# Optimization experiments

Hardware: AMD Instinct MI355X
Metric: run time of the kernel (lower is better)

The kernel has to match this reference:

```python
import jax, jax.numpy as jnp
import numpy as np

N_NODES = 50000
N_EDGES = 500000
F_IN = 16      # node feature dim F
F_OUT = 16     # channels F_
E_FEAT = 8     # edge feature dim
HIDDEN = 32    # kernel_network hidden size


def _glorot(key, shape):
    fan_in, fan_out = shape[0], shape[1]
    lim = np.sqrt(6.0 / (fan_in + fan_out)).astype(np.float32)
    return jax.random.uniform(key, shape, jnp.float32, -lim, lim)


def setup_inputs() -> dict:
    key = jax.random.key(0)
    ks = jax.random.split(key, 8)
    x = jax.random.normal(ks[0], (N_NODES, F_IN), jnp.float32)
    e = jax.random.uniform(ks[1], (N_EDGES, E_FEAT), jnp.float32)
    idx_i = jax.random.randint(ks[2], (N_EDGES,), 0, N_NODES, jnp.int32)  # targets
    idx_j = jax.random.randint(ks[3], (N_EDGES,), 0, N_NODES, jnp.int32)  # sources
    W1 = _glorot(ks[4], (E_FEAT, HIDDEN))
    b1 = jnp.zeros((HIDDEN,), jnp.float32)
    W2 = _glorot(ks[5], (HIDDEN, F_OUT * F_IN))
    b2 = jnp.zeros((F_OUT * F_IN,), jnp.float32)
    root_kernel = _glorot(ks[6], (F_IN, F_OUT))
    bias = jnp.zeros((F_OUT,), jnp.float32)
    return {"x": x, "e": e, "idx_i": idx_i, "idx_j": idx_j,
            "W1": W1, "b1": b1, "W2": W2, "b2": b2,
            "root_kernel": root_kernel, "bias": bias}


def reference(x, e, idx_i, idx_j, W1, b1, W2, b2, root_kernel, bias):
    # Edge-conditioned filter-generating network (MLP, relu hidden, linear out)
    h = jax.nn.relu(e @ W1 + b1)                       # [E, HIDDEN]
    kern = (h @ W2 + b2).reshape(-1, F_IN, F_OUT)      # [E, F, F_]
    # gather source node features, per-edge matmul, scatter-add to targets
    msg = jnp.einsum('ef,efc->ec', x[idx_j], kern)     # [E, F_]
    out = jax.ops.segment_sum(msg, idx_i, num_segments=N_NODES)  # [N, F_]
    out = out + x @ root_kernel + bias
    return out
```

## Files before the change

kernel.cpp:

```cpp
#include <hip/hip_runtime.h>

typedef __attribute__((ext_vector_type(8))) short bf16x8_t;
typedef __attribute__((ext_vector_type(4))) float f32x4_t;

__device__ __forceinline__ unsigned short f2bf(float f) {
    union { float f; unsigned int i; } v; v.f = f;
    unsigned int u = v.i;
    return (unsigned short)((u + 0x7FFFu + ((u >> 16) & 1u)) >> 16);
}

__device__ __forceinline__ unsigned int cvt_pk_bf16(float lo, float hi) {
    unsigned int r;
    asm("v_cvt_pk_bf16_f32 %0, %1, %2" : "=v"(r) : "v"(lo), "v"(hi));
    return r;
}


__global__ __launch_bounds__(256) void prep_kernel(
    const float* __restrict__ x,
    const float* __restrict__ W1,
    const float* __restrict__ b1,
    const float* __restrict__ W2,
    const float* __restrict__ b2,
    const float* __restrict__ rootk,
    const float* __restrict__ bias,
    float* __restrict__ out,
    unsigned short* __restrict__ tab,
    int n_nodes, int root_blocks)
{
    const int tid = threadIdx.x;
    const int bid = blockIdx.x;

    if (bid < root_blocks) {
        __shared__ float sR[256];
        __shared__ float sB[16];
        if (tid < 256) sR[tid] = rootk[tid];
        if (tid < 16)  sB[tid] = bias[tid];
        __syncthreads();

        int nid = bid * 256 + tid;
        if (nid >= n_nodes) return;

        const float* xp = x + (size_t)nid * 16;
        float xf[16];
#pragma unroll
        for (int f = 0; f < 16; f += 4) {
            float4 v = *reinterpret_cast<const float4*>(xp + f);
            xf[f] = v.x; xf[f + 1] = v.y; xf[f + 2] = v.z; xf[f + 3] = v.w;
        }
        float o[16];
#pragma unroll
        for (int cc = 0; cc < 16; ++cc) o[cc] = sB[cc];
#pragma unroll
        for (int f = 0; f < 16; ++f) {
            float p = xf[f];
#pragma unroll
            for (int cc = 0; cc < 16; ++cc)
                o[cc] = fmaf(p, sR[f * 16 + cc], o[cc]);
        }
        float* dst = out + (size_t)nid * 16;
#pragma unroll
        for (int cc = 0; cc < 16; cc += 4)
            *reinterpret_cast<float4*>(dst + cc) = make_float4(o[cc], o[cc+1], o[cc+2], o[cc+3]);
    } else {
        for (int it = tid; it < 64 * 19; it += 256) {
            int grp  = it >> 6;
            int lane = it & 63;
            int q = lane >> 4, cc = lane & 15;
            union { unsigned short h[8]; uint4 u; } pk;
            if (grp < 2) {
                int hh = grp;
#pragma unroll
                for (int j = 0; j < 8; ++j) {
                    float v = 0.f;
                    if (q == 0)              v = W1[j * 32 + cc + 16 * hh];
                    else if (q == 1 && j==0) v = b1[cc + 16 * hh];
                    pk.h[j] = f2bf(v);
                }
                *reinterpret_cast<uint4*>(tab + ((size_t)hh * 64 + lane) * 8) = pk.u;
            } else {
                int s = grp - 2;
#pragma unroll
                for (int j = 0; j < 8; ++j) {
                    float v;
                    if (s < 16) {
                        int hd = (j < 4) ? (4 * q + j) : (4 * q + 12 + j);
                        v = W2[hd * 256 + s * 16 + cc];
                    } else {
                        v = (q < 2) ? b2[(q * 8 + j) * 16 + cc] : 0.f;
                    }
                    pk.h[j] = f2bf(v);
                }
                *reinterpret_cast<uint4*>(tab + 1024 + ((size_t)s * 64 + lane) * 8) = pk.u;
            }
        }
    }
}

__global__ __launch_bounds__(256) void edge_mfma_kernel(
    const float* __restrict__ x,
    const float* __restrict__ efeat,
    const int*   __restrict__ idx_i,
    const int*   __restrict__ idx_j,
    const unsigned short* __restrict__ tab,
    float* __restrict__ out,
    int n_edges, int n_groups)
{
    const int lane = threadIdx.x & 63;
    const int q = lane >> 4;
    const int c = lane & 15;

    const bf16x8_t* w1f = reinterpret_cast<const bf16x8_t*>(tab) + lane;
    const bf16x8_t aW1_0 = w1f[0];
    const bf16x8_t aW1_1 = w1f[64];
    const bf16x8_t* w2f = reinterpret_cast<const bf16x8_t*>(tab + 1024) + lane;
    bf16x8_t bW2[17];
#pragma unroll
    for (int s = 0; s < 17; ++s) bW2[s] = w2f[s * 64];

    const unsigned int c1 = (q == 1) ? 0x00003F80u : 0u;
    const bool isq0 = (q == 0);
    const bool qodd = (q & 1);

    int g = blockIdx.x * 4 + (threadIdx.x >> 6);
    const int nw = gridDim.x * 4;
    if (g >= n_groups) return;

    int  eid = g * 16 + c;
    bool va  = (eid < n_edges);
    int  el  = va ? eid : (n_edges - 1);
    int  jsrc = idx_j[el];

    for (; g < n_groups; g += nw) {
        const int base = g * 16;

        const float* xp = x + (size_t)jsrc * 16;
        float4 x0 = *reinterpret_cast<const float4*>(xp);
        float4 x1 = *reinterpret_cast<const float4*>(xp + 4);
        float4 x2 = *reinterpret_cast<const float4*>(xp + 8);
        float4 x3 = *reinterpret_cast<const float4*>(xp + 12);
        const float* ep = efeat + (size_t)el * 8;
        float4 e0 = *reinterpret_cast<const float4*>(ep);
        float4 e1 = *reinterpret_cast<const float4*>(ep + 4);
        int t0, t1, t2, t3;
        if (base + 16 <= n_edges) {
            int4 tv = *reinterpret_cast<const int4*>(idx_i + base + q * 4);
            t0 = tv.x; t1 = tv.y; t2 = tv.z; t3 = tv.w;
        } else {
            const int eb = base + q * 4;
            t0 = (eb + 0 < n_edges) ? idx_i[eb + 0] : 0;
            t1 = (eb + 1 < n_edges) ? idx_i[eb + 1] : 0;
            t2 = (eb + 2 < n_edges) ? idx_i[eb + 2] : 0;
            t3 = (eb + 3 < n_edges) ? idx_i[eb + 3] : 0;
        }

        const int gn = g + nw;
        int  eidn = gn * 16 + c;
        bool van  = (eidn < n_edges);
        int  eln  = van ? eidn : (n_edges - 1);
        int  jn   = (gn < n_groups) ? idx_j[eln] : 0;

        union { bf16x8_t bf; unsigned int u[4]; } bB;
        {
            unsigned int ef0 = cvt_pk_bf16(e0.x, e0.y);
            unsigned int ef1 = cvt_pk_bf16(e0.z, e0.w);
            unsigned int ef2 = cvt_pk_bf16(e1.x, e1.y);
            unsigned int ef3 = cvt_pk_bf16(e1.z, e1.w);
            bB.u[0] = isq0 ? ef0 : c1;
            bB.u[1] = isq0 ? ef1 : 0u;
            bB.u[2] = isq0 ? ef2 : 0u;
            bB.u[3] = isq0 ? ef3 : 0u;
        }
        f32x4_t z4 = {0.f, 0.f, 0.f, 0.f};
        f32x4_t h0 = __builtin_amdgcn_mfma_f32_16x16x32_bf16(aW1_0, bB.bf, z4, 0, 0, 0);
        f32x4_t h1 = __builtin_amdgcn_mfma_f32_16x16x32_bf16(aW1_1, bB.bf, z4, 0, 0, 0);

        float hown[8];
#pragma unroll
        for (int r = 0; r < 4; ++r) {
            hown[r]     = fmaxf(h0[r], 0.f);
            hown[4 + r] = fmaxf(h1[r], 0.f);
        }

        float xf[16];
        xf[0]=x0.x; xf[1]=x0.y; xf[2]=x0.z; xf[3]=x0.w;
        xf[4]=x1.x; xf[5]=x1.y; xf[6]=x1.z; xf[7]=x1.w;
        xf[8]=x2.x; xf[9]=x2.y; xf[10]=x2.z; xf[11]=x2.w;
        xf[12]=x3.x; xf[13]=x3.y; xf[14]=x3.z; xf[15]=x3.w;
        if (!va) {
#pragma unroll
            for (int t = 0; t < 16; ++t) xf[t] = 0.f;
        }

        union { bf16x8_t bf; unsigned int u[4]; } xb;
        {
            float xs0 = qodd ? xf[8]  : xf[0];
            float xs1 = qodd ? xf[9]  : xf[1];
            float xs2 = qodd ? xf[10] : xf[2];
            float xs3 = qodd ? xf[11] : xf[3];
            float xs4 = qodd ? xf[12] : xf[4];
            float xs5 = qodd ? xf[13] : xf[5];
            float xs6 = qodd ? xf[14] : xf[6];
            float xs7 = qodd ? xf[15] : xf[7];
            xb.u[0] = cvt_pk_bf16(xs0, xs1);
            xb.u[1] = cvt_pk_bf16(xs2, xs3);
            xb.u[2] = cvt_pk_bf16(xs4, xs5);
            xb.u[3] = cvt_pk_bf16(xs6, xs7);
        }

        f32x4_t acc0 = {0.f, 0.f, 0.f, 0.f};
        f32x4_t acc1 = {0.f, 0.f, 0.f, 0.f};
        union { bf16x8_t bf; unsigned int u[4]; } afr;
#pragma unroll
        for (int s = 0; s < 16; s += 2) {
            float xs = xf[s];
            afr.u[0] = cvt_pk_bf16(hown[0] * xs, hown[1] * xs);
            afr.u[1] = cvt_pk_bf16(hown[2] * xs, hown[3] * xs);
            afr.u[2] = cvt_pk_bf16(hown[4] * xs, hown[5] * xs);
            afr.u[3] = cvt_pk_bf16(hown[6] * xs, hown[7] * xs);
            acc0 = __builtin_amdgcn_mfma_f32_16x16x32_bf16(afr.bf, bW2[s], acc0, 0, 0, 0);
            xs = xf[s + 1];
            afr.u[0] = cvt_pk_bf16(hown[0] * xs, hown[1] * xs);
            afr.u[1] = cvt_pk_bf16(hown[2] * xs, hown[3] * xs);
            afr.u[2] = cvt_pk_bf16(hown[4] * xs, hown[5] * xs);
            afr.u[3] = cvt_pk_bf16(hown[6] * xs, hown[7] * xs);
            acc1 = __builtin_amdgcn_mfma_f32_16x16x32_bf16(afr.bf, bW2[s + 1], acc1, 0, 0, 0);
        }
        acc0 = __builtin_amdgcn_mfma_f32_16x16x32_bf16(xb.bf, bW2[16], acc0, 0, 0, 0);

        const int eb = base + q * 4;
        const float r0 = acc0[0] + acc1[0];
        const float r1 = acc0[1] + acc1[1];
        const float r2 = acc0[2] + acc1[2];
        const float r3 = acc0[3] + acc1[3];
        if (eb + 0 < n_edges) atomicAdd(out + (size_t)t0 * 16 + c, r0);
        if (eb + 1 < n_edges) atomicAdd(out + (size_t)t1 * 16 + c, r1);
        if (eb + 2 < n_edges) atomicAdd(out + (size_t)t2 * 16 + c, r2);
        if (eb + 3 < n_edges) atomicAdd(out + (size_t)t3 * 16 + c, r3);

        jsrc = jn; el = eln; va = van;
    }
}

extern "C" void kernel_launch(void* const* d_in, const int* in_sizes, int n_in,
                              void* d_out, int out_size, void* d_ws, size_t ws_size,
                              hipStream_t stream) {
    const float* x     = (const float*)d_in[0];
    const float* e     = (const float*)d_in[1];
    const int*   idx_i = (const int*)d_in[2];
    const int*   idx_j = (const int*)d_in[3];
    const float* W1    = (const float*)d_in[4];
    const float* b1    = (const float*)d_in[5];
    const float* W2    = (const float*)d_in[6];
    const float* b2    = (const float*)d_in[7];
    const float* rootk = (const float*)d_in[8];
    const float* bias  = (const float*)d_in[9];

    int n_nodes  = in_sizes[0] / 16;
    int n_edges  = in_sizes[2];
    int n_groups = (n_edges + 15) / 16;

    float* out = (float*)d_out;
    unsigned short* tab = (unsigned short*)d_ws;

    int root_blocks = (n_nodes + 255) / 256;
    prep_kernel<<<root_blocks + 1, 256, 0, stream>>>(x, W1, b1, W2, b2, rootk, bias,
                                                     out, tab, n_nodes, root_blocks);

    edge_mfma_kernel<<<1024, 256, 0, stream>>>(x, e, idx_i, idx_j, tab, out,
                                               n_edges, n_groups);
}
```

Measured before the change: 46.48 us.

## Replace float atomics with per-target message slots plus gather pass

Each edge claims a slot in its target node's bucket with an integer atomic counter, then writes its 16-float message into a per-node slot buffer. A new gather kernel sums the slots into the output, and overflow beyond 48 slots falls back to float atomics. The aim is to avoid contended float atomicAdd traffic, at the cost of an extra integer atomic per edge, about 150 MB of slot writes and reads, and an extra kernel launch. The edge kernel grid is also doubled to 2048 blocks. The slot path only runs if the workspace is large enough.

```diff
diff --git a/kernel.cpp b/kernel.cpp
--- a/kernel.cpp
+++ b/kernel.cpp
@@ -2,6 +2,8 @@
 
 typedef __attribute__((ext_vector_type(8))) short bf16x8_t;
 typedef __attribute__((ext_vector_type(4))) float f32x4_t;
+
+#define SLOTS 48
 
 __device__ __forceinline__ unsigned short f2bf(float f) {
     union { float f; unsigned int i; } v; v.f = f;
@@ -26,6 +28,7 @@
     const float* __restrict__ bias,
     float* __restrict__ out,
     unsigned short* __restrict__ tab,
+    int* __restrict__ cnt,
     int n_nodes, int root_blocks)
 {
     const int tid = threadIdx.x;
@@ -40,6 +43,7 @@
 
         int nid = bid * 256 + tid;
         if (nid >= n_nodes) return;
+        if (cnt) cnt[nid] = 0;
 
         const float* xp = x + (size_t)nid * 16;
         float xf[16];
@@ -97,6 +101,7 @@
     }
 }
 
+template<int USE_SLOTS>
 __global__ __launch_bounds__(256) void edge_mfma_kernel(
     const float* __restrict__ x,
     const float* __restrict__ efeat,
@@ -104,6 +109,8 @@
     const int*   __restrict__ idx_j,
     const unsigned short* __restrict__ tab,
     float* __restrict__ out,
+    float* __restrict__ msgslot,
+    int*   __restrict__ cnt,
     int n_edges, int n_groups)
 {
     const int lane = threadIdx.x & 63;
@@ -134,14 +141,6 @@
     for (; g < n_groups; g += nw) {
         const int base = g * 16;
 
-        const float* xp = x + (size_t)jsrc * 16;
-        float4 x0 = *reinterpret_cast<const float4*>(xp);
-        float4 x1 = *reinterpret_cast<const float4*>(xp + 4);
-        float4 x2 = *reinterpret_cast<const float4*>(xp + 8);
-        float4 x3 = *reinterpret_cast<const float4*>(xp + 12);
-        const float* ep = efeat + (size_t)el * 8;
-        float4 e0 = *reinterpret_cast<const float4*>(ep);
-        float4 e1 = *reinterpret_cast<const float4*>(ep + 4);
         int t0, t1, t2, t3;
         if (base + 16 <= n_edges) {
             int4 tv = *reinterpret_cast<const int4*>(idx_i + base + q * 4);
@@ -153,6 +152,25 @@
             t2 = (eb + 2 < n_edges) ? idx_i[eb + 2] : 0;
             t3 = (eb + 3 < n_edges) ? idx_i[eb + 3] : 0;
         }
+
+        int pos_own = 0;
+        if (USE_SLOTS) {
+            int tsel = t0;
+            tsel = (c == 1) ? t1 : tsel;
+            tsel = (c == 2) ? t2 : tsel;
+            tsel = (c == 3) ? t3 : tsel;
+            if (c < 4 && (base + q * 4 + c) < n_edges)
+                pos_own = atomicAdd(cnt + tsel, 1);
+        }
+
+        const float* xp = x + (size_t)jsrc * 16;
+        float4 x0 = *reinterpret_cast<const float4*>(xp);
+        float4 x1 = *reinterpret_cast<const float4*>(xp + 4);
+        float4 x2 = *reinterpret_cast<const float4*>(xp + 8);
+        float4 x3 = *reinterpret_cast<const float4*>(xp + 12);
+        const float* ep = efeat + (size_t)el * 8;
+        float4 e0 = *reinterpret_cast<const float4*>(ep);
+        float4 e1 = *reinterpret_cast<const float4*>(ep + 4);
 
         const int gn = g + nw;
         int  eidn = gn * 16 + c;
@@ -228,18 +246,68 @@
         }
         acc0 = __builtin_amdgcn_mfma_f32_16x16x32_bf16(xb.bf, bW2[16], acc0, 0, 0, 0);
 
+        const float rr0 = acc0[0] + acc1[0];
+        const float rr1 = acc0[1] + acc1[1];
+        const float rr2 = acc0[2] + acc1[2];
+        const float rr3 = acc0[3] + acc1[3];
         const int eb = base + q * 4;
-        const float r0 = acc0[0] + acc1[0];
-        const float r1 = acc0[1] + acc1[1];
-        const float r2 = acc0[2] + acc1[2];
-        const float r3 = acc0[3] + acc1[3];
-        if (eb + 0 < n_edges) atomicAdd(out + (size_t)t0 * 16 + c, r0);
-        if (eb + 1 < n_edges) atomicAdd(out + (size_t)t1 * 16 + c, r1);
-        if (eb + 2 < n_edges) atomicAdd(out + (size_t)t2 * 16 + c, r2);
-        if (eb + 3 < n_edges) atomicAdd(out + (size_t)t3 * 16 + c, r3);
+
+        if (USE_SLOTS) {
+            const int gb = lane & 48;
+            const int p0 = __shfl(pos_own, gb + 0);
+            const int p1 = __shfl(pos_own, gb + 1);
+            const int p2 = __shfl(pos_own, gb + 2);
+            const int p3 = __shfl(pos_own, gb + 3);
+            if (eb + 0 < n_edges) {
+                if (p0 < SLOTS) msgslot[((size_t)t0 * SLOTS + p0) * 16 + c] = rr0;
+                else atomicAdd(out + (size_t)t0 * 16 + c, rr0);
+            }
+            if (eb + 1 < n_edges) {
+                if (p1 < SLOTS) msgslot[((size_t)t1 * SLOTS + p1) * 16 + c] = rr1;
+                else atomicAdd(out + (size_t)t1 * 16 + c, rr1);
+            }
+            if (eb + 2 < n_edges) {
+                if (p2 < SLOTS) msgslot[((size_t)t2 * SLOTS + p2) * 16 + c] = rr2;
+                else atomicAdd(out + (size_t)t2 * 16 + c, rr2);
+            }
+            if (eb + 3 < n_edges) {
+                if (p3 < SLOTS) msgslot[((size_t)t3 * SLOTS + p3) * 16 + c] = rr3;
+                else atomicAdd(out + (size_t)t3 * 16 + c, rr3);
+            }
+        } else {
+            if (eb + 0 < n_edges) atomicAdd(out + (size_t)t0 * 16 + c, rr0);
+            if (eb + 1 < n_edges) atomicAdd(out + (size_t)t1 * 16 + c, rr1);
+            if (eb + 2 < n_edges) atomicAdd(out + (size_t)t2 * 16 + c, rr2);
+            if (eb + 3 < n_edges) atomicAdd(out + (size_t)t3 * 16 + c, rr3);
+        }
 
         jsrc = jn; el = eln; va = van;
     }
+}
+
+__global__ __launch_bounds__(256) void gather_kernel(
+    const float* __restrict__ msgslot,
+    const int*   __restrict__ cnt,
+    float* __restrict__ out,
+    int n_nodes)
+{
+    int gi = blockIdx.x * 256 + threadIdx.x;
+    int n = gi >> 4;
+    int c = gi & 15;
+    if (n >= n_nodes) return;
+
+    int m = cnt[n];
+    m = (m < SLOTS) ? m : SLOTS;
+
+    const float* p = msgslot + (size_t)n * SLOTS * 16 + c;
+    float s0 = 0.f, s1 = 0.f;
+    int k = 0;
+    for (; k + 1 < m; k += 2) {
+        s0 += p[(size_t)k * 16];
+        s1 += p[(size_t)(k + 1) * 16];
+    }
+    if (k < m) s0 += p[(size_t)k * 16];
+    out[(size_t)n * 16 + c] += s0 + s1;
 }
 
 extern "C" void kernel_launch(void* const* d_in, const int* in_sizes, int n_in,
@@ -262,11 +330,24 @@
 
     float* out = (float*)d_out;
     unsigned short* tab = (unsigned short*)d_ws;
+    int*   cnt     = (int*)((char*)d_ws + 65536);
+    float* msgslot = (float*)((char*)d_ws + 524288);
+
+    size_t need = 524288 + (size_t)n_nodes * SLOTS * 16 * sizeof(float);
+    const int use_slots = (ws_size >= need) ? 1 : 0;
 
     int root_blocks = (n_nodes + 255) / 256;
     prep_kernel<<<root_blocks + 1, 256, 0, stream>>>(x, W1, b1, W2, b2, rootk, bias,
-                                                     out, tab, n_nodes, root_blocks);
-
-    edge_mfma_kernel<<<1024, 256, 0, stream>>>(x, e, idx_i, idx_j, tab, out,
-                                               n_edges, n_groups);
-}
+                                                     out, tab, use_slots ? cnt : nullptr,
+                                                     n_nodes, root_blocks);
+
+    if (use_slots) {
+        edge_mfma_kernel<1><<<2048, 256, 0, stream>>>(x, e, idx_i, idx_j, tab, out,
+                                                      msgslot, cnt, n_edges, n_groups);
+        int gblocks = (n_nodes * 16 + 255) / 256;
+        gather_kernel<<<gblocks, 256, 0, stream>>>(msgslot, cnt, out, n_nodes);
+    } else {
+        edge_mfma_kernel<0><<<2048, 256, 0, stream>>>(x, e, idx_i, idx_j, tab, out,
+                                                      msgslot, cnt, n_edges, n_groups);
+    }
+}
```

New measurement: 57.59 us. 23.9% more time.

## Give each wave four fixed edge groups with double-buffered gathers

Applied to the files above, without the earlier changes.

The grid-stride loop over 1024 blocks becomes a grid sized so each wave handles exactly four consecutive 16-edge groups. The source-feature and edge-feature loads for the next group are issued before the current group is computed, using two register buffers, so memory latency overlaps with MFMA work. A templated EXACT variant drops bounds checks when the edge count is a multiple of 16. This raises register pressure and launches many more blocks, and each wave's per-block setup, including loading the 17 W2 fragments, is amortised over only four groups.

```diff
diff --git a/kernel.cpp b/kernel.cpp
--- a/kernel.cpp
+++ b/kernel.cpp
@@ -14,6 +14,8 @@
     asm("v_cvt_pk_bf16_f32 %0, %1, %2" : "=v"(r) : "v"(lo), "v"(hi));
     return r;
 }
+
+#define LD4(p) (*reinterpret_cast<const float4*>(p))
 
 
 __global__ __launch_bounds__(256) void prep_kernel(
@@ -45,7 +47,7 @@
         float xf[16];
 #pragma unroll
         for (int f = 0; f < 16; f += 4) {
-            float4 v = *reinterpret_cast<const float4*>(xp + f);
+            float4 v = LD4(xp + f);
             xf[f] = v.x; xf[f + 1] = v.y; xf[f + 2] = v.z; xf[f + 3] = v.w;
         }
         float o[16];
@@ -97,6 +99,7 @@
     }
 }
 
+template<int EXACT>
 __global__ __launch_bounds__(256) void edge_mfma_kernel(
     const float* __restrict__ x,
     const float* __restrict__ efeat,
@@ -121,51 +124,44 @@
     const unsigned int c1 = (q == 1) ? 0x00003F80u : 0u;
     const bool isq0 = (q == 0);
     const bool qodd = (q & 1);
-
-    int g = blockIdx.x * 4 + (threadIdx.x >> 6);
-    const int nw = gridDim.x * 4;
-    if (g >= n_groups) return;
-
-    int  eid = g * 16 + c;
-    bool va  = (eid < n_edges);
-    int  el  = va ? eid : (n_edges - 1);
-    int  jsrc = idx_j[el];
-
-    for (; g < n_groups; g += nw) {
-        const int base = g * 16;
-
-        const float* xp = x + (size_t)jsrc * 16;
-        float4 x0 = *reinterpret_cast<const float4*>(xp);
-        float4 x1 = *reinterpret_cast<const float4*>(xp + 4);
-        float4 x2 = *reinterpret_cast<const float4*>(xp + 8);
-        float4 x3 = *reinterpret_cast<const float4*>(xp + 12);
-        const float* ep = efeat + (size_t)el * 8;
-        float4 e0 = *reinterpret_cast<const float4*>(ep);
-        float4 e1 = *reinterpret_cast<const float4*>(ep + 4);
+    float* const outc = out + c;
+
+    const int wid = blockIdx.x * 4 + (threadIdx.x >> 6);
+    const int g0  = wid * 4;
+    if (g0 >= n_groups) return;
+    const int rem = n_groups - g0;
+
+    auto ldj = [&](int gg) -> int {
+        int eid = gg * 16 + c;
+        if (!EXACT) { if (eid >= n_edges) eid = n_edges - 1; }
+        return idx_j[eid];
+    };
+    auto eoff = [&](int gg) -> size_t {
+        int eid = gg * 16 + c;
+        if (!EXACT) { if (eid >= n_edges) eid = n_edges - 1; }
+        return (size_t)eid * 8;
+    };
+
+    auto compute = [&](float4 X0, float4 X1, float4 X2, float4 X3,
+                       float4 E0, float4 E1, int gg) {
         int t0, t1, t2, t3;
-        if (base + 16 <= n_edges) {
-            int4 tv = *reinterpret_cast<const int4*>(idx_i + base + q * 4);
+        if (EXACT || (gg * 16 + 16 <= n_edges)) {
+            int4 tv = *reinterpret_cast<const int4*>(idx_i + gg * 16 + q * 4);
             t0 = tv.x; t1 = tv.y; t2 = tv.z; t3 = tv.w;
         } else {
-            const int eb = base + q * 4;
+            const int eb = gg * 16 + q * 4;
             t0 = (eb + 0 < n_edges) ? idx_i[eb + 0] : 0;
             t1 = (eb + 1 < n_edges) ? idx_i[eb + 1] : 0;
             t2 = (eb + 2 < n_edges) ? idx_i[eb + 2] : 0;
             t3 = (eb + 3 < n_edges) ? idx_i[eb + 3] : 0;
         }
 
-        const int gn = g + nw;
-        int  eidn = gn * 16 + c;
-        bool van  = (eidn < n_edges);
-        int  eln  = van ? eidn : (n_edges - 1);
-        int  jn   = (gn < n_groups) ? idx_j[eln] : 0;
-
         union { bf16x8_t bf; unsigned int u[4]; } bB;
         {
-            unsigned int ef0 = cvt_pk_bf16(e0.x, e0.y);
-            unsigned int ef1 = cvt_pk_bf16(e0.z, e0.w);
-            unsigned int ef2 = cvt_pk_bf16(e1.x, e1.y);
-            unsigned int ef3 = cvt_pk_bf16(e1.z, e1.w);
+            unsigned int ef0 = cvt_pk_bf16(E0.x, E0.y);
+            unsigned int ef1 = cvt_pk_bf16(E0.z, E0.w);
+            unsigned int ef2 = cvt_pk_bf16(E1.x, E1.y);
+            unsigned int ef3 = cvt_pk_bf16(E1.z, E1.w);
             bB.u[0] = isq0 ? ef0 : c1;
             bB.u[1] = isq0 ? ef1 : 0u;
             bB.u[2] = isq0 ? ef2 : 0u;
@@ -183,30 +179,16 @@
         }
 
         float xf[16];
-        xf[0]=x0.x; xf[1]=x0.y; xf[2]=x0.z; xf[3]=x0.w;
-        xf[4]=x1.x; xf[5]=x1.y; xf[6]=x1.z; xf[7]=x1.w;
-        xf[8]=x2.x; xf[9]=x2.y; xf[10]=x2.z; xf[11]=x2.w;
-        xf[12]=x3.x; xf[13]=x3.y; xf[14]=x3.z; xf[15]=x3.w;
-        if (!va) {
-#pragma unroll
-            for (int t = 0; t < 16; ++t) xf[t] = 0.f;
-        }
+        xf[0]=X0.x; xf[1]=X0.y; xf[2]=X0.z; xf[3]=X0.w;
+        xf[4]=X1.x; xf[5]=X1.y; xf[6]=X1.z; xf[7]=X1.w;
+        xf[8]=X2.x; xf[9]=X2.y; xf[10]=X2.z; xf[11]=X2.w;
+        xf[12]=X3.x; xf[13]=X3.y; xf[14]=X3.z; xf[15]=X3.w;
 
         union { bf16x8_t bf; unsigned int u[4]; } xb;
-        {
-            float xs0 = qodd ? xf[8]  : xf[0];
-            float xs1 = qodd ? xf[9]  : xf[1];
-            float xs2 = qodd ? xf[10] : xf[2];
-            float xs3 = qodd ? xf[11] : xf[3];
-            float xs4 = qodd ? xf[12] : xf[4];
-            float xs5 = qodd ? xf[13] : xf[5];
-            float xs6 = qodd ? xf[14] : xf[6];
-            float xs7 = qodd ? xf[15] : xf[7];
-            xb.u[0] = cvt_pk_bf16(xs0, xs1);
-            xb.u[1] = cvt_pk_bf16(xs2, xs3);
-            xb.u[2] = cvt_pk_bf16(xs4, xs5);
-            xb.u[3] = cvt_pk_bf16(xs6, xs7);
-        }
+        xb.u[0] = cvt_pk_bf16(qodd ? xf[8]  : xf[0], qodd ? xf[9]  : xf[1]);
+        xb.u[1] = cvt_pk_bf16(qodd ? xf[10] : xf[2], qodd ? xf[11] : xf[3]);
+        xb.u[2] = cvt_pk_bf16(qodd ? xf[12] : xf[4], qodd ? xf[13] : xf[5]);
+        xb.u[3] = cvt_pk_bf16(qodd ? xf[14] : xf[6], qodd ? xf[15] : xf[7]);
 
         f32x4_t acc0 = {0.f, 0.f, 0.f, 0.f};
         f32x4_t acc1 = {0.f, 0.f, 0.f, 0.f};
@@ -228,18 +210,54 @@
         }
         acc0 = __builtin_amdgcn_mfma_f32_16x16x32_bf16(xb.bf, bW2[16], acc0, 0, 0, 0);
 
-        const int eb = base + q * 4;
-        const float r0 = acc0[0] + acc1[0];
-        const float r1 = acc0[1] + acc1[1];
-        const float r2 = acc0[2] + acc1[2];
-        const float r3 = acc0[3] + acc1[3];
-        if (eb + 0 < n_edges) atomicAdd(out + (size_t)t0 * 16 + c, r0);
-        if (eb + 1 < n_edges) atomicAdd(out + (size_t)t1 * 16 + c, r1);
-        if (eb + 2 < n_edges) atomicAdd(out + (size_t)t2 * 16 + c, r2);
-        if (eb + 3 < n_edges) atomicAdd(out + (size_t)t3 * 16 + c, r3);
-
-        jsrc = jn; el = eln; va = van;
+        const float rr0 = acc0[0] + acc1[0];
+        const float rr1 = acc0[1] + acc1[1];
+        const float rr2 = acc0[2] + acc1[2];
+        const float rr3 = acc0[3] + acc1[3];
+        if (EXACT) {
+            atomicAdd(outc + (size_t)t0 * 16, rr0);
+            atomicAdd(outc + (size_t)t1 * 16, rr1);
+            atomicAdd(outc + (size_t)t2 * 16, rr2);
+            atomicAdd(outc + (size_t)t3 * 16, rr3);
+        } else {
+            const int eb = gg * 16 + q * 4;
+            if (eb + 0 < n_edges) atomicAdd(outc + (size_t)t0 * 16, rr0);
+            if (eb + 1 < n_edges) atomicAdd(outc + (size_t)t1 * 16, rr1);
+            if (eb + 2 < n_edges) atomicAdd(outc + (size_t)t2 * 16, rr2);
+            if (eb + 3 < n_edges) atomicAdd(outc + (size_t)t3 * 16, rr3);
+        }
+    };
+
+#define STAGE(B0,B1,B2,B3,BE0,BE1, jv, gg)                         \
+    {                                                              \
+        const float* xp = x + (size_t)(jv) * 16;                   \
+        B0 = LD4(xp); B1 = LD4(xp + 4);                            \
+        B2 = LD4(xp + 8); B3 = LD4(xp + 12);                       \
+        const float* ep = efeat + eoff(gg);                        \
+        BE0 = LD4(ep); BE1 = LD4(ep + 4);                          \
     }
+
+    const int jA = ldj(g0);
+    const int jB = (rem > 1) ? ldj(g0 + 1) : 0;
+    const int jC = (rem > 2) ? ldj(g0 + 2) : 0;
+    const int jD = (rem > 3) ? ldj(g0 + 3) : 0;
+
+    float4 a0, a1, a2, a3, ae0, ae1;
+    float4 b0, b1, b2, b3, be0, be1;
+
+    STAGE(a0,a1,a2,a3,ae0,ae1, jA, g0);
+    if (rem > 1) STAGE(b0,b1,b2,b3,be0,be1, jB, g0 + 1);
+    compute(a0,a1,a2,a3,ae0,ae1, g0);
+    if (rem > 1) {
+        if (rem > 2) STAGE(a0,a1,a2,a3,ae0,ae1, jC, g0 + 2);
+        compute(b0,b1,b2,b3,be0,be1, g0 + 1);
+        if (rem > 2) {
+            if (rem > 3) STAGE(b0,b1,b2,b3,be0,be1, jD, g0 + 3);
+            compute(a0,a1,a2,a3,ae0,ae1, g0 + 2);
+            if (rem > 3) compute(b0,b1,b2,b3,be0,be1, g0 + 3);
+        }
+    }
+#undef STAGE
 }
 
 extern "C" void kernel_launch(void* const* d_in, const int* in_sizes, int n_in,
@@ -267,6 +285,11 @@
     prep_kernel<<<root_blocks + 1, 256, 0, stream>>>(x, W1, b1, W2, b2, rootk, bias,
                                                      out, tab, n_nodes, root_blocks);
 
-    edge_mfma_kernel<<<1024, 256, 0, stream>>>(x, e, idx_i, idx_j, tab, out,
-                                               n_edges, n_groups);
-}
+    int blocks = (n_groups + 15) / 16;
+    if ((n_edges & 15) == 0)
+        edge_mfma_kernel<1><<<blocks, 256, 0, stream>>>(x, e, idx_i, idx_j, tab, out,
+                                                        n_edges, n_groups);
+    else
+        edge_mfma_kernel<0><<<blocks, 256, 0, stream>>>(x, e, idx_i, idx_j, tab, out,
+                                                        n_edges, n_groups);
+}
```

After: 44.23 us. 4.9% less time.
